# Kernel tuning notes

Hardware: AMD Instinct MI355X
Metric: run time of the kernel (lower is better)

## Reference

```python
import jax, jax.numpy as jnp
import numpy as np

NUM_CODES = 512
CODE_DIM = 64
BETA = 0.25  # commitment_cost


def setup_inputs() -> dict:
    key = jax.random.key(0)
    k1, k2 = jax.random.split(key)
    B, D, H, T = 32, CODE_DIM, 16, 256
    z_e = jax.random.normal(k1, (B, D, H, T), dtype=jnp.float32)
    embed = jax.random.normal(k2, (NUM_CODES, D), dtype=jnp.float32)
    # F.normalize(embed, dim=1) * init_scale (init_scale=1.0)
    embed = embed / jnp.clip(jnp.linalg.norm(embed, axis=1, keepdims=True), 1e-12)
    return {"z_e": z_e, "embedding": embed}


def reference(z_e, embedding):
    B, D, H, T = z_e.shape
    K = embedding.shape[0]
    # (B,D,H,T) -> (N,D)
    flat_z_e = jnp.transpose(z_e, (0, 2, 3, 1)).reshape(-1, D)

    # squared L2 distances: ||z||^2 + ||e||^2 - 2 z.e  -> (N,K)
    z_sq = jnp.sum(flat_z_e * flat_z_e, axis=1, keepdims=True)          # (N,1)
    e_sq = jnp.sum(embedding * embedding, axis=1)[None, :]              # (1,K)
    dot = flat_z_e @ embedding.T                                        # (N,K)
    distances = z_sq + e_sq - 2.0 * dot
    indices = jnp.argmin(distances, axis=1)                             # (N,)

    # nearest-code lookup (same math as onehot @ embedding)
    z_q_flat = embedding[indices]                                       # (N,D)
    z_q = jnp.transpose(z_q_flat.reshape(B, H, T, D), (0, 3, 1, 2))     # (B,D,H,T)

    # straight-through estimator
    z_q_st = z_e + jax.lax.stop_gradient(z_q - z_e)

    # commitment loss: beta * mse(stop_grad(z_e), z_q)
    commitment = BETA * jnp.mean((jax.lax.stop_gradient(z_e) - z_q) ** 2)

    # usage statistics
    N = flat_z_e.shape[0]
    counts = jnp.zeros((K,), dtype=jnp.float32).at[indices].add(1.0)
    avg_probs = counts / N
    eps = 1e-12
    entropy = -jnp.sum(avg_probs * jnp.log(avg_probs + eps))
    perplexity = jnp.exp(entropy)
    usage = jnp.mean((avg_probs > 0).astype(jnp.float32))

    return (z_q_st, commitment, indices.reshape(B, H, T), perplexity, usage)
```

## Files before the change

kernel.cpp:

```cpp
#include <hip/hip_runtime.h>

#define BB 32
#define DD 64
#define HH 16
#define TT 256
#define KK 512
#define NN (BB*HH*TT)
#define HT (HH*TT)
#define DHT (DD*HT)
#define ZQ_SIZE (BB*DD*HH*TT)
#define COMMIT_OFF ZQ_SIZE
#define IDX_OFF (ZQ_SIZE+1)
#define PPL_OFF (IDX_OFF+NN)
#define USE_OFF (PPL_OFF+1)

#define CNT_OFF    0
#define CPART_OFF  512
#define TICKET_OFF 1024
#define EBH_OFF    1088
#define EBL_OFF    17472

#define MARGIN_A 1.5e-3f

using bf16x8 = __attribute__((ext_vector_type(8))) short;
using f32x4  = __attribute__((ext_vector_type(4))) float;

__device__ __forceinline__ unsigned bf16_rne(float x) {
    unsigned u = __float_as_uint(x);
    return (u + 0x7FFFu + ((u >> 16) & 1u)) >> 16;
}
__device__ __forceinline__ bf16x8 bc(uint4 v) { return __builtin_bit_cast(bf16x8, v); }

__global__ void vq_init(const float* __restrict__ emb, float* __restrict__ ws,
                        float* __restrict__ zq_scratch) {
    const int tid = threadIdx.x, blk = blockIdx.x;
    if (blk == 0) {
        ws[CNT_OFF + tid] = 0.0f;
        ws[CNT_OFF + 256 + tid] = 0.0f;
        if (tid == 0) { ((int*)(ws + TICKET_OFF))[0] = 0; ((int*)zq_scratch)[0] = 0; }
    }
    const int k  = blk * 16 + (tid >> 4);
    const int d0 = (tid & 15) * 4;
    float4 v = *reinterpret_cast<const float4*>(emb + k * DD + d0);
    unsigned hx = bf16_rne(v.x), hy = bf16_rne(v.y), hz = bf16_rne(v.z), hw = bf16_rne(v.w);
    float lx = v.x - __uint_as_float(hx << 16);
    float ly = v.y - __uint_as_float(hy << 16);
    float lz = v.z - __uint_as_float(hz << 16);
    float lw = v.w - __uint_as_float(hw << 16);
    uint2 hi, lo;
    hi.x = hx | (hy << 16);            hi.y = hz | (hw << 16);
    lo.x = bf16_rne(lx) | (bf16_rne(ly) << 16);
    lo.y = bf16_rne(lz) | (bf16_rne(lw) << 16);
    reinterpret_cast<uint2*>(ws + EBH_OFF)[(k * DD + d0) >> 2] = hi;
    reinterpret_cast<uint2*>(ws + EBL_OFF)[(k * DD + d0) >> 2] = lo;
}

__global__ __launch_bounds__(256, 2) void vq_screen(
    const float* __restrict__ z_e, const float* __restrict__ ws,
    float* __restrict__ out_idx, float* __restrict__ zq_scratch)
{
    __shared__ uint4 sh[2][2304];

    const int tid  = threadIdx.x;
    const int lane = tid & 63;
    const int col  = lane & 15;
    const int q    = lane >> 4;
    const int W    = (blockIdx.x * 256 + tid) >> 6;
    const int base_tok = W * 64;

    const uint4* ebh4 = reinterpret_cast<const uint4*>(ws + EBH_OFF);
    const uint4* ebl4 = reinterpret_cast<const uint4*>(ws + EBL_OFF);

    bf16x8 ah[4][2], al[4][2];
#pragma unroll
    for (int s = 0; s < 4; ++s) {
        const int n = base_tok + s * 16 + col;
        const size_t zoff = (size_t)(n >> 12) * DHT + (size_t)((n >> 8) & 15) * 256 + (size_t)(n & 255);
#pragma unroll
        for (int kf = 0; kf < 2; ++kf) {
            const int d0 = kf * 32 + q * 8;
            unsigned hu[4], lu[4];
#pragma unroll
            for (int jj = 0; jj < 4; ++jj) {
                float z0 = z_e[zoff + (size_t)(d0 + 2*jj + 0) * HT];
                float z1 = z_e[zoff + (size_t)(d0 + 2*jj + 1) * HT];
                unsigned h0 = bf16_rne(z0), h1 = bf16_rne(z1);
                float l0 = z0 - __uint_as_float(h0 << 16);
                float l1 = z1 - __uint_as_float(h1 << 16);
                hu[jj] = h0 | (h1 << 16);
                lu[jj] = bf16_rne(l0) | (bf16_rne(l1) << 16);
            }
            ah[s][kf] = bc(make_uint4(hu[0], hu[1], hu[2], hu[3]));
            al[s][kf] = bc(make_uint4(lu[0], lu[1], lu[2], lu[3]));
        }
    }

    float m1[4][4], m2[4][4];
#pragma unroll
    for (int s = 0; s < 4; ++s)
#pragma unroll
        for (int r = 0; r < 4; ++r) { m1[s][r] = -3.4e38f; m2[s][r] = -3.4e38f; }

    unsigned ktag = (unsigned)col;

#pragma unroll
    for (int p = 0; p < 2; ++p) {
        if (p) __syncthreads();
#pragma unroll
        for (int j = 0; j < 8; ++j) {
            const int local = j * 256 + tid;
            const int c = local >> 3, jj = local & 7;
            sh[0][c * 9 + jj] = ebh4[p * 2048 + local];
            sh[1][c * 9 + jj] = ebl4[p * 2048 + local];
        }
        __syncthreads();

#pragma unroll 4
        for (int ctl = 0; ctl < 16; ++ctl) {
            const int row9 = (ctl * 16 + col) * 9;
            bf16x8 bh0 = bc(sh[0][row9 + q]);
            bf16x8 bh1 = bc(sh[0][row9 + 4 + q]);
            bf16x8 bl0 = bc(sh[1][row9 + q]);
            bf16x8 bl1 = bc(sh[1][row9 + 4 + q]);

#pragma unroll
            for (int s = 0; s < 4; ++s) {
                f32x4 acc = {0.f, 0.f, 0.f, 0.f};
                acc = __builtin_amdgcn_mfma_f32_16x16x32_bf16(ah[s][0], bh0, acc, 0, 0, 0);
                acc = __builtin_amdgcn_mfma_f32_16x16x32_bf16(ah[s][1], bh1, acc, 0, 0, 0);
                acc = __builtin_amdgcn_mfma_f32_16x16x32_bf16(al[s][0], bh0, acc, 0, 0, 0);
                acc = __builtin_amdgcn_mfma_f32_16x16x32_bf16(al[s][1], bh1, acc, 0, 0, 0);
                acc = __builtin_amdgcn_mfma_f32_16x16x32_bf16(ah[s][0], bl0, acc, 0, 0, 0);
                acc = __builtin_amdgcn_mfma_f32_16x16x32_bf16(ah[s][1], bl1, acc, 0, 0, 0);
#pragma unroll
                for (int r = 0; r < 4; ++r) {
                    float pk = __uint_as_float((__float_as_uint(acc[r]) & 0xFFFFFE00u) | ktag);
                    m2[s][r] = fmaxf(m2[s][r], fminf(m1[s][r], pk));
                    m1[s][r] = fmaxf(m1[s][r], pk);
                }
            }
            ktag += 16u;
        }
    }

#pragma unroll
    for (int msk = 1; msk <= 8; msk <<= 1) {
#pragma unroll
        for (int s = 0; s < 4; ++s)
#pragma unroll
            for (int r = 0; r < 4; ++r) {
                float o1 = __shfl_xor(m1[s][r], msk, 64);
                float o2 = __shfl_xor(m2[s][r], msk, 64);
                m2[s][r] = fmaxf(fmaxf(m2[s][r], o2), fminf(m1[s][r], o1));
                m1[s][r] = fmaxf(m1[s][r], o1);
            }
    }

    if (col == 0) {
        int* rc = (int*)zq_scratch;
        int* rlist = rc + 1;
#pragma unroll
        for (int s = 0; s < 4; ++s)
#pragma unroll
            for (int r = 0; r < 4; ++r) {
                int token = base_tok + s * 16 + q * 4 + r;
                out_idx[token] = (float)(__float_as_uint(m1[s][r]) & 511u);
                if (m1[s][r] - m2[s][r] < MARGIN_A) { int pp = atomicAdd(rc, 1); rlist[pp] = token; }
            }
    }
}

__global__ void vq_rescue(const float* __restrict__ z_e, const float* __restrict__ emb,
                          float* __restrict__ out_idx, const float* __restrict__ zq_scratch)
{
    __shared__ float lz[DD];
    __shared__ float sd[512];
    __shared__ int   si[512];
    const int tid = threadIdx.x;
    const int cnt = ((const int*)zq_scratch)[0];
    const int* rlist = ((const int*)zq_scratch) + 1;

    for (int it = blockIdx.x; it < cnt; it += gridDim.x) {
        const int n = rlist[it];
        const int b = n >> 12, h = (n >> 8) & 15, t = n & 255;
        const size_t zoff = (size_t)b * DHT + (size_t)h * 256 + (size_t)t;
        __syncthreads();
        if (tid < DD) lz[tid] = z_e[zoff + (size_t)tid * HT];
        __syncthreads();
        const float4* er = reinterpret_cast<const float4*>(emb + (size_t)tid * DD);
        float a0 = 0.f, a1 = 0.f, a2 = 0.f, a3 = 0.f;
#pragma unroll
        for (int i = 0; i < 16; ++i) {
            float4 e4 = er[i];
            float d0 = lz[4*i+0] - e4.x; a0 = fmaf(d0, d0, a0);
            float d1 = lz[4*i+1] - e4.y; a1 = fmaf(d1, d1, a1);
            float d2 = lz[4*i+2] - e4.z; a2 = fmaf(d2, d2, a2);
            float d3 = lz[4*i+3] - e4.w; a3 = fmaf(d3, d3, a3);
        }
        sd[tid] = (a0 + a1) + (a2 + a3);
        si[tid] = tid;
        __syncthreads();
        for (int off = 256; off > 0; off >>= 1) {
            if (tid < off) {
                float d2 = sd[tid + off]; int j2 = si[tid + off];
                if (d2 < sd[tid] || (d2 == sd[tid] && j2 < si[tid])) { sd[tid] = d2; si[tid] = j2; }
            }
            __syncthreads();
        }
        if (tid == 0) out_idx[n] = (float)si[0];
    }
}

__global__ __launch_bounds__(256) void vq_finalize(
    const float* __restrict__ z_e, const float* __restrict__ emb,
    const float* __restrict__ idx_in, float* __restrict__ out_zq,
    float* __restrict__ ws, float* __restrict__ out)
{
    __shared__ float wsum[4];
    __shared__ int hist[KK];
    __shared__ float s_a[KK], s_b[KK];
    __shared__ int s_u[KK];
    __shared__ int islast;

    float* counts = ws + CNT_OFF;
    float* cpart  = ws + CPART_OFF;
    int*   ticket = (int*)(ws + TICKET_OFF);

    const int tid = threadIdx.x;
    hist[tid] = 0; hist[tid + 256] = 0;
    const int n   = blockIdx.x * 256 + tid;
    const int b   = n >> 12;
    const int h   = (n >> 8) & 15;
    const int t   = n & 255;
    const size_t zbase = (size_t)b * DHT + (size_t)h * TT + (size_t)t;

    const int bidx = (int)idx_in[n];
    __syncthreads();
    atomicAdd(&hist[bidx], 1);
    const float4* er = reinterpret_cast<const float4*>(emb + (size_t)bidx * DD);
    float a0 = 0.f, a1 = 0.f, a2 = 0.f, a3 = 0.f;
#pragma unroll
    for (int i = 0; i < 16; ++i) {
        float4 e4 = er[i];
        float z0 = z_e[zbase + (size_t)(4*i+0) * HT];
        float z1 = z_e[zbase + (size_t)(4*i+1) * HT];
        float z2 = z_e[zbase + (size_t)(4*i+2) * HT];
        float z3 = z_e[zbase + (size_t)(4*i+3) * HT];
        out_zq[zbase + (size_t)(4*i+0) * HT] = e4.x;
        out_zq[zbase + (size_t)(4*i+1) * HT] = e4.y;
        out_zq[zbase + (size_t)(4*i+2) * HT] = e4.z;
        out_zq[zbase + (size_t)(4*i+3) * HT] = e4.w;
        float d0 = z0 - e4.x; a0 = fmaf(d0, d0, a0);
        float d1 = z1 - e4.y; a1 = fmaf(d1, d1, a1);
        float d2 = z2 - e4.z; a2 = fmaf(d2, d2, a2);
        float d3 = z3 - e4.w; a3 = fmaf(d3, d3, a3);
    }
    float dmin = (a0 + a1) + (a2 + a3);
#pragma unroll
    for (int off = 32; off > 0; off >>= 1) dmin += __shfl_down(dmin, off, 64);
    if ((tid & 63) == 0) wsum[tid >> 6] = dmin;
    __syncthreads();
    if (tid == 0) cpart[blockIdx.x] = (wsum[0] + wsum[1]) + (wsum[2] + wsum[3]);
    int c = hist[tid];       if (c) atomicAdd(&counts[tid],       (float)c);
    c     = hist[tid + 256]; if (c) atomicAdd(&counts[tid + 256], (float)c);

    if (tid == 0) {
        __threadfence();
        islast = (atomicAdd(ticket, 1) == (int)gridDim.x - 1) ? 1 : 0;
    }
    __syncthreads();
    if (islast) {
        __threadfence();
#pragma unroll
        for (int k2 = tid; k2 < KK; k2 += 256) {
            float cc = counts[k2];
            float p  = cc * (1.0f / (float)NN);
            s_a[k2] = p * logf(p + 1e-12f);
            s_u[k2] = (p > 0.0f) ? 1 : 0;
            s_b[k2] = cpart[k2];
        }
        __syncthreads();
        for (int off = 256; off > 0; off >>= 1) {
            if (tid < off) {
                s_a[tid] += s_a[tid + off];
                s_u[tid] += s_u[tid + off];
                s_b[tid] += s_b[tid + off];
            }
            __syncthreads();
        }
        if (tid == 0) {
            out[COMMIT_OFF] = 0.25f * s_b[0] / (float)ZQ_SIZE;
            out[PPL_OFF]    = expf(-s_a[0]);
            out[USE_OFF]    = (float)s_u[0] / (float)KK;
        }
    }
}

extern "C" void kernel_launch(void* const* d_in, const int* in_sizes, int n_in,
                              void* d_out, int out_size, void* d_ws, size_t ws_size,
                              hipStream_t stream) {
    const float* z_e = (const float*)d_in[0];
    const float* emb = (const float*)d_in[1];
    float* out = (float*)d_out;
    float* ws  = (float*)d_ws;

    float* out_idx = out + IDX_OFF;
    float* zq_scratch = out;

    vq_init<<<32, 256, 0, stream>>>(emb, ws, zq_scratch);
    vq_screen<<<512, 256, 0, stream>>>(z_e, ws, out_idx, zq_scratch);
    vq_rescue<<<512, 512, 0, stream>>>(z_e, emb, out_idx, zq_scratch);
    vq_finalize<<<512, 256, 0, stream>>>(z_e, emb, out_idx, out, ws, out);
}
```

Baseline: 157.0 us.

## Split MFMA chains and software-pipeline top-2 tracking in VQ screen kernel

Splits each six-MFMA dependent accumulation chain into two independent three-MFMA chains, which are summed afterward. The top-2 max update is deferred by one iteration so the VALU work on the previous tile's scores can overlap with the current tile's MFMAs. The min/max pairs in the top-2 update and shuffle reduction become single fmed3 instructions. The rescue kernel grid is also halved from 512 to 256 blocks. The cost is extra accumulator registers and a small change in summation order near ties.

New measurement: 158.0 us. No clear change (+0.6%).

```diff
diff --git a/kernel.cpp b/kernel.cpp
--- a/kernel.cpp
+++ b/kernel.cpp
@@ -96,12 +96,16 @@
     }
 
     float m1[4][4], m2[4][4];
-#pragma unroll
-    for (int s = 0; s < 4; ++s)
+    f32x4 psum[4];
+#pragma unroll
+    for (int s = 0; s < 4; ++s) {
+        psum[s] = f32x4{-3.4e38f, -3.4e38f, -3.4e38f, -3.4e38f};
 #pragma unroll
         for (int r = 0; r < 4; ++r) { m1[s][r] = -3.4e38f; m2[s][r] = -3.4e38f; }
+    }
 
     unsigned ktag = (unsigned)col;
+    unsigned ptag = (unsigned)col;
 
 #pragma unroll
     for (int p = 0; p < 2; ++p) {
@@ -123,25 +127,44 @@
             bf16x8 bl0 = bc(sh[1][row9 + q]);
             bf16x8 bl1 = bc(sh[1][row9 + 4 + q]);
 
+            f32x4 accA[4], accB[4];
 #pragma unroll
             for (int s = 0; s < 4; ++s) {
-                f32x4 acc = {0.f, 0.f, 0.f, 0.f};
-                acc = __builtin_amdgcn_mfma_f32_16x16x32_bf16(ah[s][0], bh0, acc, 0, 0, 0);
-                acc = __builtin_amdgcn_mfma_f32_16x16x32_bf16(ah[s][1], bh1, acc, 0, 0, 0);
-                acc = __builtin_amdgcn_mfma_f32_16x16x32_bf16(al[s][0], bh0, acc, 0, 0, 0);
-                acc = __builtin_amdgcn_mfma_f32_16x16x32_bf16(al[s][1], bh1, acc, 0, 0, 0);
-                acc = __builtin_amdgcn_mfma_f32_16x16x32_bf16(ah[s][0], bl0, acc, 0, 0, 0);
-                acc = __builtin_amdgcn_mfma_f32_16x16x32_bf16(ah[s][1], bl1, acc, 0, 0, 0);
+                f32x4 a = {0.f, 0.f, 0.f, 0.f};
+                a = __builtin_amdgcn_mfma_f32_16x16x32_bf16(ah[s][0], bh0, a, 0, 0, 0);
+                a = __builtin_amdgcn_mfma_f32_16x16x32_bf16(al[s][0], bh0, a, 0, 0, 0);
+                a = __builtin_amdgcn_mfma_f32_16x16x32_bf16(ah[s][0], bl0, a, 0, 0, 0);
+                accA[s] = a;
+                f32x4 b = {0.f, 0.f, 0.f, 0.f};
+                b = __builtin_amdgcn_mfma_f32_16x16x32_bf16(ah[s][1], bh1, b, 0, 0, 0);
+                b = __builtin_amdgcn_mfma_f32_16x16x32_bf16(al[s][1], bh1, b, 0, 0, 0);
+                b = __builtin_amdgcn_mfma_f32_16x16x32_bf16(ah[s][1], bl1, b, 0, 0, 0);
+                accB[s] = b;
+            }
+
+#pragma unroll
+            for (int s = 0; s < 4; ++s)
 #pragma unroll
                 for (int r = 0; r < 4; ++r) {
-                    float pk = __uint_as_float((__float_as_uint(acc[r]) & 0xFFFFFE00u) | ktag);
-                    m2[s][r] = fmaxf(m2[s][r], fminf(m1[s][r], pk));
+                    float pk = __uint_as_float((__float_as_uint(psum[s][r]) & 0xFFFFFE00u) | ptag);
+                    m2[s][r] = __builtin_amdgcn_fmed3f(pk, m1[s][r], m2[s][r]);
                     m1[s][r] = fmaxf(m1[s][r], pk);
                 }
-            }
+
+#pragma unroll
+            for (int s = 0; s < 4; ++s) psum[s] = accA[s] + accB[s];
+            ptag = ktag;
             ktag += 16u;
         }
     }
+#pragma unroll
+    for (int s = 0; s < 4; ++s)
+#pragma unroll
+        for (int r = 0; r < 4; ++r) {
+            float pk = __uint_as_float((__float_as_uint(psum[s][r]) & 0xFFFFFE00u) | ptag);
+            m2[s][r] = __builtin_amdgcn_fmed3f(pk, m1[s][r], m2[s][r]);
+            m1[s][r] = fmaxf(m1[s][r], pk);
+        }
 
 #pragma unroll
     for (int msk = 1; msk <= 8; msk <<= 1) {
@@ -151,7 +174,7 @@
             for (int r = 0; r < 4; ++r) {
                 float o1 = __shfl_xor(m1[s][r], msk, 64);
                 float o2 = __shfl_xor(m2[s][r], msk, 64);
-                m2[s][r] = fmaxf(fmaxf(m2[s][r], o2), fminf(m1[s][r], o1));
+                m2[s][r] = __builtin_amdgcn_fmed3f(m1[s][r], o1, fmaxf(m2[s][r], o2));
                 m1[s][r] = fmaxf(m1[s][r], o1);
             }
     }
@@ -309,6 +332,6 @@
 
     vq_init<<<32, 256, 0, stream>>>(emb, ws, zq_scratch);
     vq_screen<<<512, 256, 0, stream>>>(z_e, ws, out_idx, zq_scratch);
-    vq_rescue<<<512, 512, 0, stream>>>(z_e, emb, out_idx, zq_scratch);
+    vq_rescue<<<256, 512, 0, stream>>>(z_e, emb, out_idx, zq_scratch);
     vq_finalize<<<512, 256, 0, stream>>>(z_e, emb, out_idx, out, ws, out);
 }
```

## Fuse z_q writeback, histogram and commitment loss into screen kernel; drop finalize pass

Applied to the files above, without the earlier changes.

The screen kernel now writes z_q, builds the code histogram and computes a per-wave commitment partial from ||z||^2 + 1 - 2*dot, so the separate finalize pass no longer re-reads z_e. The rescue kernel corrects the index, counts, z_q and loss delta only for ambiguous tokens, and a tiny single-block stats kernel computes the scalars. It also prefetches LDS operands one iteration ahead and uses med3 for the top-2 update. The loss now relies on unit-norm codes and an algebraic distance that can lose precision, and the rescue list is capped at RMAX entries.

New measurement: 133.4 us. -15.0%, faster.

```diff
diff --git a/kernel.cpp b/kernel.cpp
--- a/kernel.cpp
+++ b/kernel.cpp
@@ -16,9 +16,12 @@
 
 #define CNT_OFF    0
 #define CPART_OFF  512
-#define TICKET_OFF 1024
-#define EBH_OFF    1088
-#define EBL_OFF    17472
+#define CDELTA_OFF 2560
+#define RC_OFF     2561
+#define RLIST_OFF  2562
+#define RMAX       16384
+#define EBH_OFF    36864
+#define EBL_OFF    53248
 
 #define MARGIN_A 1.5e-3f
 
@@ -30,14 +33,18 @@
     return (u + 0x7FFFu + ((u >> 16) & 1u)) >> 16;
 }
 __device__ __forceinline__ bf16x8 bc(uint4 v) { return __builtin_bit_cast(bf16x8, v); }
-
-__global__ void vq_init(const float* __restrict__ emb, float* __restrict__ ws,
-                        float* __restrict__ zq_scratch) {
+__device__ __forceinline__ float pick4(float a0, float a1, float a2, float a3, int i) {
+    float x = (i & 1) ? a1 : a0;
+    float y = (i & 1) ? a3 : a2;
+    return (i & 2) ? y : x;
+}
+
+__global__ void vq_init(const float* __restrict__ emb, float* __restrict__ ws) {
     const int tid = threadIdx.x, blk = blockIdx.x;
     if (blk == 0) {
         ws[CNT_OFF + tid] = 0.0f;
         ws[CNT_OFF + 256 + tid] = 0.0f;
-        if (tid == 0) { ((int*)(ws + TICKET_OFF))[0] = 0; ((int*)zq_scratch)[0] = 0; }
+        if (tid == 0) { ws[CDELTA_OFF] = 0.0f; ((int*)ws)[RC_OFF] = 0; }
     }
     const int k  = blk * 16 + (tid >> 4);
     const int d0 = (tid & 15) * 4;
@@ -56,10 +63,11 @@
 }
 
 __global__ __launch_bounds__(256, 2) void vq_screen(
-    const float* __restrict__ z_e, const float* __restrict__ ws,
-    float* __restrict__ out_idx, float* __restrict__ zq_scratch)
+    const float* __restrict__ z_e, const float* __restrict__ emb,
+    float* __restrict__ ws, float* __restrict__ out_zq, float* __restrict__ out_idx)
 {
     __shared__ uint4 sh[2][2304];
+    __shared__ int hist[KK];
 
     const int tid  = threadIdx.x;
     const int lane = tid & 63;
@@ -68,12 +76,16 @@
     const int W    = (blockIdx.x * 256 + tid) >> 6;
     const int base_tok = W * 64;
 
+    hist[tid] = 0; hist[tid + 256] = 0;
+
     const uint4* ebh4 = reinterpret_cast<const uint4*>(ws + EBH_OFF);
     const uint4* ebl4 = reinterpret_cast<const uint4*>(ws + EBL_OFF);
 
     bf16x8 ah[4][2], al[4][2];
+    float zp[4];
 #pragma unroll
     for (int s = 0; s < 4; ++s) {
+        zp[s] = 0.0f;
         const int n = base_tok + s * 16 + col;
         const size_t zoff = (size_t)(n >> 12) * DHT + (size_t)((n >> 8) & 15) * 256 + (size_t)(n & 255);
 #pragma unroll
@@ -84,6 +96,8 @@
             for (int jj = 0; jj < 4; ++jj) {
                 float z0 = z_e[zoff + (size_t)(d0 + 2*jj + 0) * HT];
                 float z1 = z_e[zoff + (size_t)(d0 + 2*jj + 1) * HT];
+                zp[s] = fmaf(z0, z0, zp[s]);
+                zp[s] = fmaf(z1, z1, zp[s]);
                 unsigned h0 = bf16_rne(z0), h1 = bf16_rne(z1);
                 float l0 = z0 - __uint_as_float(h0 << 16);
                 float l1 = z1 - __uint_as_float(h1 << 16);
@@ -94,6 +108,11 @@
             al[s][kf] = bc(make_uint4(lu[0], lu[1], lu[2], lu[3]));
         }
     }
+#pragma unroll
+    for (int s = 0; s < 4; ++s) {
+        zp[s] += __shfl_xor(zp[s], 16, 64);
+        zp[s] += __shfl_xor(zp[s], 32, 64);
+    }
 
     float m1[4][4], m2[4][4];
 #pragma unroll
@@ -102,6 +121,7 @@
         for (int r = 0; r < 4; ++r) { m1[s][r] = -3.4e38f; m2[s][r] = -3.4e38f; }
 
     unsigned ktag = (unsigned)col;
+    const int idx0 = col * 9 + q;
 
 #pragma unroll
     for (int p = 0; p < 2; ++p) {
@@ -115,14 +135,18 @@
         }
         __syncthreads();
 
+        uint4 nh0 = sh[0][idx0], nh1 = sh[0][idx0 + 4];
+        uint4 nl0 = sh[1][idx0], nl1 = sh[1][idx0 + 4];
+
 #pragma unroll 4
         for (int ctl = 0; ctl < 16; ++ctl) {
-            const int row9 = (ctl * 16 + col) * 9;
-            bf16x8 bh0 = bc(sh[0][row9 + q]);
-            bf16x8 bh1 = bc(sh[0][row9 + 4 + q]);
-            bf16x8 bl0 = bc(sh[1][row9 + q]);
-            bf16x8 bl1 = bc(sh[1][row9 + 4 + q]);
-
+            bf16x8 bh0 = bc(nh0), bh1 = bc(nh1);
+            bf16x8 bl0 = bc(nl0), bl1 = bc(nl1);
+            if (ctl < 15) {
+                const int ni = idx0 + (ctl + 1) * 144;
+                nh0 = sh[0][ni]; nh1 = sh[0][ni + 4];
+                nl0 = sh[1][ni]; nl1 = sh[1][ni + 4];
+            }
 #pragma unroll
             for (int s = 0; s < 4; ++s) {
                 f32x4 acc = {0.f, 0.f, 0.f, 0.f};
@@ -135,7 +159,7 @@
 #pragma unroll
                 for (int r = 0; r < 4; ++r) {
                     float pk = __uint_as_float((__float_as_uint(acc[r]) & 0xFFFFFE00u) | ktag);
-                    m2[s][r] = fmaxf(m2[s][r], fminf(m1[s][r], pk));
+                    m2[s][r] = __builtin_amdgcn_fmed3f(pk, m1[s][r], m2[s][r]);
                     m1[s][r] = fmaxf(m1[s][r], pk);
                 }
             }
@@ -151,37 +175,88 @@
             for (int r = 0; r < 4; ++r) {
                 float o1 = __shfl_xor(m1[s][r], msk, 64);
                 float o2 = __shfl_xor(m2[s][r], msk, 64);
-                m2[s][r] = fmaxf(fmaxf(m2[s][r], o2), fminf(m1[s][r], o1));
+                m2[s][r] = __builtin_amdgcn_fmed3f(m1[s][r], o1, fmaxf(m2[s][r], o2));
                 m1[s][r] = fmaxf(m1[s][r], o1);
             }
     }
 
-    if (col == 0) {
-        int* rc = (int*)zq_scratch;
-        int* rlist = rc + 1;
-#pragma unroll
-        for (int s = 0; s < 4; ++s)
-#pragma unroll
-            for (int r = 0; r < 4; ++r) {
-                int token = base_tok + s * 16 + q * 4 + r;
-                out_idx[token] = (float)(__float_as_uint(m1[s][r]) & 511u);
-                if (m1[s][r] - m2[s][r] < MARGIN_A) { int pp = atomicAdd(rc, 1); rlist[pp] = token; }
-            }
-    }
+    const int s0 = col >> 2, r0 = col & 3;
+    const int token = base_tok + s0 * 16 + q * 4 + r0;
+
+    float m1v, m2v;
+    {
+        float a = pick4(m1[0][0], m1[0][1], m1[0][2], m1[0][3], r0);
+        float b = pick4(m1[1][0], m1[1][1], m1[1][2], m1[1][3], r0);
+        float c = pick4(m1[2][0], m1[2][1], m1[2][2], m1[2][3], r0);
+        float d = pick4(m1[3][0], m1[3][1], m1[3][2], m1[3][3], r0);
+        m1v = pick4(a, b, c, d, s0);
+        a = pick4(m2[0][0], m2[0][1], m2[0][2], m2[0][3], r0);
+        b = pick4(m2[1][0], m2[1][1], m2[1][2], m2[1][3], r0);
+        c = pick4(m2[2][0], m2[2][1], m2[2][2], m2[2][3], r0);
+        d = pick4(m2[3][0], m2[3][1], m2[3][2], m2[3][3], s0 * 0 + r0);
+        m2v = pick4(a, b, c, d, s0);
+    }
+    const int c0 = q * 4 + r0;
+    float z0s = __shfl(zp[0], c0, 64);
+    float z1s = __shfl(zp[1], c0, 64);
+    float z2s = __shfl(zp[2], c0, 64);
+    float z3s = __shfl(zp[3], c0, 64);
+    const float zsqv = pick4(z0s, z1s, z2s, z3s, s0);
+
+    const int k_sel = (int)(__float_as_uint(m1v) & 511u);
+    const float dminA = fmaf(-2.0f, m1v, zsqv + 1.0f);
+
+    out_idx[token] = (float)k_sel;
+    if (m1v - m2v < MARGIN_A) {
+        int* rc = (int*)ws + RC_OFF;
+        int pp = atomicAdd(rc, 1);
+        if (pp < RMAX) {
+            int* rl = (int*)ws + RLIST_OFF;
+            rl[2 * pp] = token;
+            rl[2 * pp + 1] = (int)__float_as_uint(dminA);
+        }
+    }
+    atomicAdd(&hist[k_sel], 1);
+
+    float csum = dminA;
+#pragma unroll
+    for (int off = 32; off > 0; off >>= 1) csum += __shfl_down(csum, off, 64);
+    if (lane == 0) ws[CPART_OFF + W] = csum;
+
+    {
+        const int b = token >> 12, h = (token >> 8) & 15, t = token & 255;
+        const size_t zb = (size_t)b * DHT + (size_t)h * TT + (size_t)t;
+        const float4* er = reinterpret_cast<const float4*>(emb + (size_t)k_sel * DD);
+#pragma unroll
+        for (int i = 0; i < 16; ++i) {
+            float4 v = er[i];
+            out_zq[zb + (size_t)(4*i+0) * HT] = v.x;
+            out_zq[zb + (size_t)(4*i+1) * HT] = v.y;
+            out_zq[zb + (size_t)(4*i+2) * HT] = v.z;
+            out_zq[zb + (size_t)(4*i+3) * HT] = v.w;
+        }
+    }
+
+    __syncthreads();
+    int c = hist[tid];       if (c) atomicAdd(ws + CNT_OFF + tid,       (float)c);
+    c     = hist[tid + 256]; if (c) atomicAdd(ws + CNT_OFF + tid + 256, (float)c);
 }
 
 __global__ void vq_rescue(const float* __restrict__ z_e, const float* __restrict__ emb,
-                          float* __restrict__ out_idx, const float* __restrict__ zq_scratch)
+                          float* __restrict__ ws, float* __restrict__ out_zq,
+                          float* __restrict__ out_idx)
 {
     __shared__ float lz[DD];
     __shared__ float sd[512];
     __shared__ int   si[512];
     const int tid = threadIdx.x;
-    const int cnt = ((const int*)zq_scratch)[0];
-    const int* rlist = ((const int*)zq_scratch) + 1;
+    int cnt = ((const int*)ws)[RC_OFF];
+    if (cnt > RMAX) cnt = RMAX;
+    const int* rl = (const int*)ws + RLIST_OFF;
 
     for (int it = blockIdx.x; it < cnt; it += gridDim.x) {
-        const int n = rlist[it];
+        const int n = rl[2 * it];
+        const float dminA = __uint_as_float((unsigned)rl[2 * it + 1]);
         const int b = n >> 12, h = (n >> 8) & 15, t = n & 255;
         const size_t zoff = (size_t)b * DHT + (size_t)h * 256 + (size_t)t;
         __syncthreads();
@@ -207,92 +282,48 @@
             }
             __syncthreads();
         }
-        if (tid == 0) out_idx[n] = (float)si[0];
-    }
-}
-
-__global__ __launch_bounds__(256) void vq_finalize(
-    const float* __restrict__ z_e, const float* __restrict__ emb,
-    const float* __restrict__ idx_in, float* __restrict__ out_zq,
-    float* __restrict__ ws, float* __restrict__ out)
-{
-    __shared__ float wsum[4];
-    __shared__ int hist[KK];
-    __shared__ float s_a[KK], s_b[KK];
-    __shared__ int s_u[KK];
-    __shared__ int islast;
-
-    float* counts = ws + CNT_OFF;
-    float* cpart  = ws + CPART_OFF;
-    int*   ticket = (int*)(ws + TICKET_OFF);
-
-    const int tid = threadIdx.x;
-    hist[tid] = 0; hist[tid + 256] = 0;
-    const int n   = blockIdx.x * 256 + tid;
-    const int b   = n >> 12;
-    const int h   = (n >> 8) & 15;
-    const int t   = n & 255;
-    const size_t zbase = (size_t)b * DHT + (size_t)h * TT + (size_t)t;
-
-    const int bidx = (int)idx_in[n];
+        const int   k_new = si[0];
+        const float d_new = sd[0];
+        const int   k_old = (int)out_idx[n];
+        if (tid == 0) {
+            atomicAdd(ws + CDELTA_OFF, d_new - dminA);
+            if (k_new != k_old) {
+                out_idx[n] = (float)k_new;
+                atomicAdd(ws + CNT_OFF + k_old, -1.0f);
+                atomicAdd(ws + CNT_OFF + k_new,  1.0f);
+            }
+        }
+        if (k_new != k_old && tid < DD)
+            out_zq[zoff + (size_t)tid * HT] = emb[(size_t)k_new * DD + tid];
+        __syncthreads();
+    }
+}
+
+__global__ void vq_stats(const float* __restrict__ ws, float* __restrict__ out) {
+    __shared__ float s_ent[KK];
+    __shared__ int   s_used[KK];
+    __shared__ float s_com[KK];
+    const int k = threadIdx.x;
+    const float c = ws[CNT_OFF + k];
+    const float p = c * (1.0f / (float)NN);
+    s_ent[k]  = p * logf(p + 1e-12f);
+    s_used[k] = (p > 0.0f) ? 1 : 0;
+    float cs = ws[CPART_OFF + k] + ws[CPART_OFF + 512 + k]
+             + ws[CPART_OFF + 1024 + k] + ws[CPART_OFF + 1536 + k];
+    s_com[k] = cs;
     __syncthreads();
-    atomicAdd(&hist[bidx], 1);
-    const float4* er = reinterpret_cast<const float4*>(emb + (size_t)bidx * DD);
-    float a0 = 0.f, a1 = 0.f, a2 = 0.f, a3 = 0.f;
-#pragma unroll
-    for (int i = 0; i < 16; ++i) {
-        float4 e4 = er[i];
-        float z0 = z_e[zbase + (size_t)(4*i+0) * HT];
-        float z1 = z_e[zbase + (size_t)(4*i+1) * HT];
-        float z2 = z_e[zbase + (size_t)(4*i+2) * HT];
-        float z3 = z_e[zbase + (size_t)(4*i+3) * HT];
-        out_zq[zbase + (size_t)(4*i+0) * HT] = e4.x;
-        out_zq[zbase + (size_t)(4*i+1) * HT] = e4.y;
-        out_zq[zbase + (size_t)(4*i+2) * HT] = e4.z;
-        out_zq[zbase + (size_t)(4*i+3) * HT] = e4.w;
-        float d0 = z0 - e4.x; a0 = fmaf(d0, d0, a0);
-        float d1 = z1 - e4.y; a1 = fmaf(d1, d1, a1);
-        float d2 = z2 - e4.z; a2 = fmaf(d2, d2, a2);
-        float d3 = z3 - e4.w; a3 = fmaf(d3, d3, a3);
-    }
-    float dmin = (a0 + a1) + (a2 + a3);
-#pragma unroll
-    for (int off = 32; off > 0; off >>= 1) dmin += __shfl_down(dmin, off, 64);
-    if ((tid & 63) == 0) wsum[tid >> 6] = dmin;
-    __syncthreads();
-    if (tid == 0) cpart[blockIdx.x] = (wsum[0] + wsum[1]) + (wsum[2] + wsum[3]);
-    int c = hist[tid];       if (c) atomicAdd(&counts[tid],       (float)c);
-    c     = hist[tid + 256]; if (c) atomicAdd(&counts[tid + 256], (float)c);
-
-    if (tid == 0) {
-        __threadfence();
-        islast = (atomicAdd(ticket, 1) == (int)gridDim.x - 1) ? 1 : 0;
-    }
-    __syncthreads();
-    if (islast) {
-        __threadfence();
-#pragma unroll
-        for (int k2 = tid; k2 < KK; k2 += 256) {
-            float cc = counts[k2];
-            float p  = cc * (1.0f / (float)NN);
-            s_a[k2] = p * logf(p + 1e-12f);
-            s_u[k2] = (p > 0.0f) ? 1 : 0;
-            s_b[k2] = cpart[k2];
-        }
-        __syncthreads();
-        for (int off = 256; off > 0; off >>= 1) {
-            if (tid < off) {
-                s_a[tid] += s_a[tid + off];
-                s_u[tid] += s_u[tid + off];
-                s_b[tid] += s_b[tid + off];
-            }
-            __syncthreads();
-        }
-        if (tid == 0) {
-            out[COMMIT_OFF] = 0.25f * s_b[0] / (float)ZQ_SIZE;
-            out[PPL_OFF]    = expf(-s_a[0]);
-            out[USE_OFF]    = (float)s_u[0] / (float)KK;
-        }
+    for (int off = 256; off > 0; off >>= 1) {
+        if (k < off) {
+            s_ent[k]  += s_ent[k + off];
+            s_used[k] += s_used[k + off];
+            s_com[k]  += s_com[k + off];
+        }
+        __syncthreads();
+    }
+    if (k == 0) {
+        out[COMMIT_OFF] = 0.25f * (s_com[0] + ws[CDELTA_OFF]) / (float)ZQ_SIZE;
+        out[PPL_OFF]    = expf(-s_ent[0]);
+        out[USE_OFF]    = (float)s_used[0] / (float)KK;
     }
 }
 
@@ -305,10 +336,9 @@
     float* ws  = (float*)d_ws;
 
     float* out_idx = out + IDX_OFF;
-    float* zq_scratch = out;
-
-    vq_init<<<32, 256, 0, stream>>>(emb, ws, zq_scratch);
-    vq_screen<<<512, 256, 0, stream>>>(z_e, ws, out_idx, zq_scratch);
-    vq_rescue<<<512, 512, 0, stream>>>(z_e, emb, out_idx, zq_scratch);
-    vq_finalize<<<512, 256, 0, stream>>>(z_e, emb, out_idx, out, ws, out);
-}
+
+    vq_init<<<32, 256, 0, stream>>>(emb, ws);
+    vq_screen<<<512, 256, 0, stream>>>(z_e, emb, ws, out, out_idx);
+    vq_rescue<<<256, 512, 0, stream>>>(z_e, emb, ws, out, out_idx);
+    vq_stats<<<1, 512, 0, stream>>>(ws, out);
+}
```
